# Kernel optimization log

Measured on AMD Instinct MI355X. Metric: run time of the kernel, lower is better.

The kernel has to match this reference:

```python
import jax, jax.numpy as jnp
import numpy as np
from jax import lax

B, CIN, COUT, H, W, K = 256, 512, 256, 8, 8, 8192


def setup_inputs() -> dict:
    key = jax.random.key(0)
    ks = jax.random.split(key, 6)
    scale = 0.05
    return {
        "latent": jax.random.normal(ks[0], (B, CIN, H, W), dtype=jnp.float32),
        "conv_w": jax.random.normal(ks[1], (COUT, CIN, 3, 3), dtype=jnp.float32) * scale,
        "conv_b": jax.random.normal(ks[2], (COUT,), dtype=jnp.float32) * scale,
        "lin_w": jax.random.normal(ks[3], (COUT, COUT), dtype=jnp.float32) * scale,
        "lin_b": jax.random.normal(ks[4], (COUT,), dtype=jnp.float32) * scale,
        "emb": jax.random.normal(ks[5], (K, COUT), dtype=jnp.float32),
    }


def reference(latent, conv_w, conv_b, lin_w, lin_b, emb):
    # pre-quantization conv: 3x3, stride 1, padding 1 (SAME), NCHW / OIHW
    x = lax.conv_general_dilated(
        latent, conv_w, window_strides=(1, 1), padding="SAME",
        dimension_numbers=("NCHW", "OIHW", "NCHW"),
    ) + conv_b[None, :, None, None]
    # permute(0,2,3,1) then linear on last dim
    x = jnp.transpose(x, (0, 2, 3, 1))              # [B,H,W,C]
    x = jnp.einsum("bhwc,dc->bhwd", x, lin_w) + lin_b
    flat = x.reshape(-1, x.shape[-1])               # [B*H*W, C]
    distances = (
        jnp.sum(flat ** 2, axis=1, keepdims=True)
        + jnp.sum(emb ** 2, axis=1)
        - 2.0 * flat @ emb.T
    )                                               # [B*H*W, K]
    encoding_indices = jnp.argmin(distances, axis=1)
    return encoding_indices.reshape(-1, 64)
```

## Files before the change

### kernel.cpp

```cpp
#include <hip/hip_runtime.h>
#include <cstdint>
#include <cstddef>


#define CIN_  512
#define E_    4608
#define M_    16384

typedef _Float16 half4_t __attribute__((ext_vector_type(4)));
typedef _Float16 half8_t __attribute__((ext_vector_type(8)));
typedef float f32x4 __attribute__((ext_vector_type(4)));

#define GLOAD_LDS16(gptr, lptr)                                         \
    __builtin_amdgcn_global_load_lds(                                   \
        (const __attribute__((address_space(1))) unsigned int*)(gptr),  \
        (__attribute__((address_space(3))) unsigned int*)(lptr), 16, 0, 0)

__global__ __launch_bounds__(256) void prep_k(
    const float* __restrict__ lat, const float* __restrict__ lin_w,
    const float* __restrict__ conv_w, const float* __restrict__ conv_b,
    const float* __restrict__ lin_b,
    _Float16* __restrict__ Xnp, _Float16* __restrict__ W2x,
    float* __restrict__ b2) {
    __shared__ float ls[8448];
    int bb = blockIdx.x, t = threadIdx.x;

    if (bb < 256) {
        float (*lt)[65] = (float(*)[65])ls;
        const float* src = lat + (size_t)bb * 512 * 64;
        _Float16* dst = Xnp + (size_t)bb * 64 * 1024;
        for (int c0 = 0; c0 < 512; c0 += 128) {
            __syncthreads();
            #pragma unroll
            for (int j = 0; j < 8; ++j) {
                int f4 = t + j * 256;
                int cc = f4 >> 4, p4 = (f4 & 15) * 4;
                float4 v = *(const float4*)(src + (size_t)(c0 + cc) * 64 + p4);
                lt[cc][p4] = v.x; lt[cc][p4 + 1] = v.y;
                lt[cc][p4 + 2] = v.z; lt[cc][p4 + 3] = v.w;
            }
            __syncthreads();
            int pix = t >> 2, cr = (t & 3) * 32;
            #pragma unroll
            for (int q = 0; q < 4; ++q) {
                half8_t hh, ll;
                #pragma unroll
                for (int j = 0; j < 8; ++j) {
                    float v = lt[cr + q * 8 + j][pix];
                    _Float16 h = (_Float16)v;
                    hh[j] = h; ll[j] = (_Float16)(v - (float)h);
                }
                *(half8_t*)(dst + (size_t)pix * 1024 + c0 + cr + q * 8) = hh;
                *(half8_t*)(dst + (size_t)pix * 1024 + 512 + c0 + cr + q * 8) = ll;
            }
        }
    } else if (bb < 832) {
        float (*lw)[33] = (float(*)[33])ls;
        int e0 = (bb - 256) * 8;
        int d = t;
        float acc[8];
        #pragma unroll
        for (int j = 0; j < 8; ++j) acc[j] = 0.f;
        for (int c0 = 0; c0 < 256; c0 += 32) {
            __syncthreads();
            #pragma unroll
            for (int k = 0; k < 8; ++k) {
                int f4 = t + k * 256;
                int row = f4 >> 3, c4 = (f4 & 7) * 4;
                float4 v = *(const float4*)(lin_w + (size_t)row * 256 + c0 + c4);
                lw[row][c4] = v.x; lw[row][c4 + 1] = v.y;
                lw[row][c4 + 2] = v.z; lw[row][c4 + 3] = v.w;
            }
            __syncthreads();
            for (int cp = 0; cp < 32; ++cp) {
                float lwv = lw[d][cp];
                const float* cwr = conv_w + (size_t)(c0 + cp) * E_ + e0;
                #pragma unroll
                for (int j = 0; j < 8; ++j) acc[j] += cwr[j] * lwv;
            }
        }
        #pragma unroll
        for (int j = 0; j < 8; ++j) {
            int e = e0 + j;
            int c = e / 9, t9 = e - c * 9;
            _Float16 h = (_Float16)acc[j];
            _Float16 l = (_Float16)(acc[j] - (float)h);
            W2x[((size_t)(t9 * 256 + d)) * 512 + c] = h;
            W2x[((size_t)((9 + t9) * 256 + d)) * 512 + c] = l;
        }
    } else {
        float (*lw)[33] = (float(*)[33])ls;
        int d = t;
        float acc = lin_b[d];
        for (int c0 = 0; c0 < 256; c0 += 32) {
            __syncthreads();
            #pragma unroll
            for (int k = 0; k < 8; ++k) {
                int f4 = t + k * 256;
                int row = f4 >> 3, c4 = (f4 & 7) * 4;
                float4 v = *(const float4*)(lin_w + (size_t)row * 256 + c0 + c4);
                lw[row][c4] = v.x; lw[row][c4 + 1] = v.y;
                lw[row][c4 + 2] = v.z; lw[row][c4 + 3] = v.w;
            }
            __syncthreads();
            for (int cp = 0; cp < 32; ++cp) acc += lw[d][cp] * conv_b[c0 + cp];
        }
        b2[d] = acc;
    }
}

__global__ __launch_bounds__(256) void convm8_k(
    const _Float16* __restrict__ Xnp, const _Float16* __restrict__ W2x,
    const float* __restrict__ b2, float* __restrict__ yb,
    float* __restrict__ tmp) {
    __shared__ char sm[65536];
    int m0 = blockIdx.x * 128, n0 = blockIdx.y * 128;
    int cc0 = blockIdx.z * 8;
    int tid = threadIdx.x, w = tid >> 6, lane = tid & 63;
    int wm = w & 1, wn = w >> 1;
    int fr = lane & 15, fq = lane >> 4;

    int xq = (fq ^ ((fr >> 1) & 3)) << 4;
    int boff[4];
    #pragma unroll
    for (int i = 0; i < 4; ++i) boff[i] = (wn * 64 + i * 16 + fr) * 64 + xq;
    int imgoff[4], ph[4], pw[4];
    #pragma unroll
    for (int s = 0; s < 4; ++s) {
        int rr = wm * 64 + s * 16 + fr;
        imgoff[s] = rr & 64; ph[s] = (rr >> 3) & 7; pw[s] = rr & 7;
    }
    int slt[2], sr[2], sq[2];
    #pragma unroll
    for (int i = 0; i < 2; ++i) {
        int s = w * 128 + i * 64 + lane;
        slt[i] = s;
        sr[i] = s >> 2;
        sq[i] = ((s & 3) ^ ((s >> 3) & 3)) * 8;
    }

    auto stageA = [&](int cc, int buf) {
        char* L = sm + buf * 16384;
        #pragma unroll
        for (int i = 0; i < 2; ++i) {
            const _Float16* base =
                Xnp + (size_t)(m0 + sr[i]) * 1024 + cc * 32 + sq[i];
            GLOAD_LDS16(base, L + slt[i] * 16);
            GLOAD_LDS16(base + 512, L + 8192 + slt[i] * 16);
        }
    };
    auto stageB = [&](int tap, int cc, int buf) {
        char* L = sm + 32768 + buf * 16384;
        #pragma unroll
        for (int i = 0; i < 2; ++i) {
            const _Float16* bb =
                W2x + ((size_t)(tap * 256 + n0 + sr[i])) * 512 + cc * 32 + sq[i];
            GLOAD_LDS16(bb, L + slt[i] * 16);
            GLOAD_LDS16(bb + (size_t)9 * 256 * 512, L + 8192 + slt[i] * 16);
        }
    };

    f32x4 acc[4][4];
    #pragma unroll
    for (int s = 0; s < 4; ++s)
        #pragma unroll
        for (int t = 0; t < 4; ++t)
            #pragma unroll
            for (int r = 0; r < 4; ++r) acc[s][t][r] = 0.f;

    stageA(cc0, 0);
    stageB(0, cc0, 0);
    const half8_t zfrag = {};
    int gi = 0;
    for (int cci = 0; cci < 8; ++cci) {
        int cc = cc0 + cci;
        const char* Ab = sm + (cci & 1) * 16384;
        for (int tap = 0; tap < 9; ++tap, ++gi) {
            __syncthreads();
            if (tap < 8) stageB(tap + 1, cc, (gi + 1) & 1);
            else if (cci < 7) stageB(0, cc + 1, (gi + 1) & 1);
            if (tap == 7 && cci < 7) stageA(cc + 1, (cci + 1) & 1);

            int dy = tap / 3 - 1, dx = tap - (tap / 3) * 3 - 1;
            half8_t ah[4], al[4];
            #pragma unroll
            for (int s = 0; s < 4; ++s) {
                int ih = ph[s] + dy, iw = pw[s] + dx;
                bool v = ((unsigned)ih < 8u) && ((unsigned)iw < 8u);
                int pp = imgoff[s] + (v ? ih * 8 + iw : 0);
                int ao = pp * 64 + ((fq ^ ((pp >> 1) & 3)) << 4);
                half8_t a0 = *(const half8_t*)(Ab + ao);
                half8_t a1 = *(const half8_t*)(Ab + 8192 + ao);
                ah[s] = v ? a0 : zfrag;
                al[s] = v ? a1 : zfrag;
            }
            const char* Bb = sm + 32768 + (gi & 1) * 16384;
            half8_t bh[4], bl[4];
            #pragma unroll
            for (int t = 0; t < 4; ++t) {
                bh[t] = *(const half8_t*)(Bb + boff[t]);
                bl[t] = *(const half8_t*)(Bb + 8192 + boff[t]);
            }
            #pragma unroll
            for (int s = 0; s < 4; ++s)
                #pragma unroll
                for (int t = 0; t < 4; ++t)
                    acc[s][t] = __builtin_amdgcn_mfma_f32_16x16x32_f16(
                        ah[s], bh[t], acc[s][t], 0, 0, 0);
            #pragma unroll
            for (int s = 0; s < 4; ++s)
                #pragma unroll
                for (int t = 0; t < 4; ++t)
                    acc[s][t] = __builtin_amdgcn_mfma_f32_16x16x32_f16(
                        ah[s], bl[t], acc[s][t], 0, 0, 0);
            #pragma unroll
            for (int s = 0; s < 4; ++s)
                #pragma unroll
                for (int t = 0; t < 4; ++t)
                    acc[s][t] = __builtin_amdgcn_mfma_f32_16x16x32_f16(
                        al[s], bh[t], acc[s][t], 0, 0, 0);
        }
    }

    float* dst = (blockIdx.z == 0) ? yb : tmp;
    float bv[4];
    #pragma unroll
    for (int t = 0; t < 4; ++t)
        bv[t] = (blockIdx.z == 0) ? b2[n0 + wn * 64 + t * 16 + fr] : 0.f;
    #pragma unroll
    for (int s = 0; s < 4; ++s)
        #pragma unroll
        for (int r = 0; r < 4; ++r) {
            int m = m0 + wm * 64 + s * 16 + fq * 4 + r;
            #pragma unroll
            for (int t = 0; t < 4; ++t) {
                int d = n0 + wn * 64 + t * 16 + fr;
                dst[(size_t)m * 256 + d] = acc[s][t][r] + bv[t];
            }
        }
}

__global__ __launch_bounds__(256) void pack3_k(
    float* __restrict__ yb, const float* __restrict__ tmp,
    const float* __restrict__ emb,
    _Float16* __restrict__ A2, _Float16* __restrict__ B2,
    float* __restrict__ esq) {
    #pragma unroll
    for (int it = 0; it < 8; ++it) {
        int i = (blockIdx.x + it * 512) * 256 + threadIdx.x;
        float4 v = *(const float4*)(yb + (size_t)i * 4);
        float4 t = *(const float4*)(tmp + (size_t)i * 4);
        float4 s = {v.x + t.x, v.y + t.y, v.z + t.z, v.w + t.w};
        *(float4*)(yb + (size_t)i * 4) = s;
        half4_t h = {(_Float16)s.x, (_Float16)s.y, (_Float16)s.z, (_Float16)s.w};
        *(half4_t*)(A2 + (size_t)i * 4) = h;
    }
    int w = threadIdx.x >> 6, lane = threadIdx.x & 63;
    #pragma unroll
    for (int j = 0; j < 4; ++j) {
        int k = blockIdx.x * 16 + w * 4 + j;
        float4 v = *(const float4*)(emb + (size_t)k * 256 + lane * 4);
        half4_t h = {(_Float16)v.x, (_Float16)v.y, (_Float16)v.z, (_Float16)v.w};
        *(half4_t*)(B2 + (size_t)k * 256 + lane * 4) = h;
        float s = v.x * v.x + v.y * v.y + v.z * v.z + v.w * v.w;
        #pragma unroll
        for (int m = 32; m >= 1; m >>= 1) s += __shfl_xor(s, m, 64);
        if (lane == 0) esq[k] = s;
    }
}

__global__ __launch_bounds__(512) void screen11_k(
    const _Float16* __restrict__ A2, const _Float16* __restrict__ B2,
    const float* __restrict__ esq, float* __restrict__ ps2, int* __restrict__ pi2) {
    __shared__ char sm[49152];
    int Lb = blockIdx.x;
    int xcd = Lb & 7, j = Lb >> 3;
    int mt = xcd * 16 + (j & 15);
    int nt = j >> 4;
    int m0 = mt * 128, n0 = nt * 256;
    int tid = threadIdx.x, w = tid >> 6, lane = tid & 63;
    int wm = w & 1, wn = w >> 1;
    int fr = lane & 15, fq = lane >> 4;

    int xq = (fq ^ ((fr >> 1) & 3)) << 4;
    int aoff[4], boff[4];
    #pragma unroll
    for (int i = 0; i < 4; ++i) {
        aoff[i] = (wm * 64 + i * 16 + fr) * 64 + xq;
        boff[i] = (wn * 64 + i * 16 + fr) * 64 + xq;
    }
    int sAr = tid >> 2, sAq = ((tid & 3) ^ ((tid >> 3) & 3)) * 8;
    int sBs[2], sBr[2], sBq[2];
    #pragma unroll
    for (int i = 0; i < 2; ++i) {
        int s = i * 512 + tid;
        sBs[i] = s;
        sBr[i] = s >> 2;
        sBq[i] = ((s & 3) ^ ((s >> 3) & 3)) * 8;
    }

    auto stage = [&](int kt, int buf) {
        char* L = sm + buf * 24576;
        int ko = kt * 32;
        GLOAD_LDS16(A2 + (size_t)(m0 + sAr) * 256 + ko + sAq, L + tid * 16);
        #pragma unroll
        for (int i = 0; i < 2; ++i)
            GLOAD_LDS16(B2 + (size_t)(n0 + sBr[i]) * 256 + ko + sBq[i],
                        L + 8192 + sBs[i] * 16);
    };

    f32x4 acc[4][4];
    #pragma unroll
    for (int s = 0; s < 4; ++s)
        #pragma unroll
        for (int t = 0; t < 4; ++t)
            #pragma unroll
            for (int r = 0; r < 4; ++r) acc[s][t][r] = 0.f;

    stage(0, 0);
    for (int kt = 0; kt < 8; ++kt) {
        __syncthreads();
        if (kt + 1 < 8) stage(kt + 1, (kt + 1) & 1);
        const char* L = sm + (kt & 1) * 24576;
        half8_t af[4], bf[4];
        #pragma unroll
        for (int s = 0; s < 4; ++s) af[s] = *(const half8_t*)(L + aoff[s]);
        #pragma unroll
        for (int t = 0; t < 4; ++t) bf[t] = *(const half8_t*)(L + 8192 + boff[t]);
        #pragma unroll
        for (int s = 0; s < 4; ++s)
            #pragma unroll
            for (int t = 0; t < 4; ++t)
                acc[s][t] = __builtin_amdgcn_mfma_f32_16x16x32_f16(
                    af[s], bf[t], acc[s][t], 0, 0, 0);
    }

    float esv[4];
    #pragma unroll
    for (int t = 0; t < 4; ++t) esv[t] = esq[n0 + wn * 64 + t * 16 + fr];
    int colIdx = nt * 4 + wn;
    #pragma unroll
    for (int s = 0; s < 4; ++s) {
        #pragma unroll
        for (int r = 0; r < 4; ++r) {
            float best = 3.4e38f; int bidx = 0x7fffffff;
            #pragma unroll
            for (int t = 0; t < 4; ++t) {
                float sc = esv[t] - 2.f * acc[s][t][r];
                int k = n0 + wn * 64 + t * 16 + fr;
                if (sc < best || (sc == best && k < bidx)) { best = sc; bidx = k; }
            }
            #pragma unroll
            for (int msk = 1; msk <= 8; msk <<= 1) {
                float so = __shfl_xor(best, msk, 64);
                int ko2 = __shfl_xor(bidx, msk, 64);
                if (so < best || (so == best && ko2 < bidx)) { best = so; bidx = ko2; }
            }
            if (fr == 0) {
                int m = m0 + wm * 64 + s * 16 + fq * 4 + r;
                ps2[(size_t)m * 128 + colIdx] = best;
                pi2[(size_t)m * 128 + colIdx] = bidx;
            }
        }
    }
}

__global__ __launch_bounds__(256) void refine3_k(
    const float* __restrict__ y, const float* __restrict__ emb,
    const float* __restrict__ esq, const float* __restrict__ ps2,
    const int* __restrict__ pi2, int* __restrict__ out) {
    int lane = threadIdx.x & 63;
    for (int j = 0; j < 8; ++j) {
        int m = blockIdx.x * 32 + j * 4 + (threadIdx.x >> 6);
        float4 yv = *(const float4*)(y + (size_t)m * 256 + lane * 4);
        float sc_[2]; int kc_[2];
        #pragma unroll
        for (int i = 0; i < 2; ++i) {
            sc_[i] = ps2[(size_t)m * 128 + lane * 2 + i];
            kc_[i] = pi2[(size_t)m * 128 + lane * 2 + i];
        }
        float s0 = fminf(sc_[0], sc_[1]);
        #pragma unroll
        for (int msk = 1; msk <= 32; msk <<= 1) s0 = fminf(s0, __shfl_xor(s0, msk, 64));
        float thr = s0 + 0.25f;
        float best = 3.4e38f; int bk = 0x7fffffff;
        for (int c = 0; c < 128; ++c) {
            float scc = __shfl(sc_[c & 1], c >> 1, 64);
            if (scc <= thr) {
                int k = __shfl(kc_[c & 1], c >> 1, 64);
                float4 ev = *(const float4*)(emb + (size_t)k * 256 + lane * 4);
                float d = yv.x * ev.x + yv.y * ev.y + yv.z * ev.z + yv.w * ev.w;
                #pragma unroll
                for (int msk = 1; msk <= 32; msk <<= 1) d += __shfl_xor(d, msk, 64);
                float sx = esq[k] - 2.f * d;
                if (sx < best || (sx == best && k < bk)) { best = sx; bk = k; }
            }
        }
        if (lane == 0) out[m] = bk;
    }
}

extern "C" void kernel_launch(void* const* d_in, const int* in_sizes, int n_in,
                              void* d_out, int out_size, void* d_ws, size_t ws_size,
                              hipStream_t stream) {
    const float* latent = (const float*)d_in[0];
    const float* conv_w = (const float*)d_in[1];
    const float* conv_b = (const float*)d_in[2];
    const float* lin_w  = (const float*)d_in[3];
    const float* lin_b  = (const float*)d_in[4];
    const float* emb    = (const float*)d_in[5];
    int* out = (int*)d_out;

    char* W = (char*)d_ws;
    float*    b2  = (float*)(W + 262144);
    float*    esq = (float*)(W + 263168);
    float*    yb  = (float*)(W + 295936);
    _Float16* W2x = (_Float16*)(W + 17073152);
    _Float16* Xnp = (_Float16*)(W + 21792768);
    _Float16* A2  = (_Float16*)(W + 21792768);
    _Float16* B2  = (_Float16*)(W + 30181376);
    float*    ps2 = (float*)(W + 34375680);
    int*      pi2 = (int*)(W + 42764288);
    float*    tmp = (float*)(W + 34375680);

    prep_k<<<833, 256, 0, stream>>>(latent, lin_w, conv_w, conv_b, lin_b,
                                    Xnp, W2x, b2);
    convm8_k<<<dim3(128, 2, 2), 256, 0, stream>>>(Xnp, W2x, b2, yb, tmp);
    pack3_k<<<512, 256, 0, stream>>>(yb, tmp, emb, A2, B2, esq);
    screen11_k<<<4096, 512, 0, stream>>>(A2, B2, esq, ps2, pi2);
    refine3_k<<<512, 256, 0, stream>>>(yb, emb, esq, ps2, pi2, out);
}
```

Before: 440.3 us.

## Merge conv N-tiles into 512-thread blocks sharing A tile; split screen launch

```diff
diff --git a/kernel.cpp b/kernel.cpp
--- a/kernel.cpp
+++ b/kernel.cpp
@@ -109,15 +109,16 @@
     }
 }
 
-__global__ __launch_bounds__(256) void convm8_k(
+__global__ __launch_bounds__(512) void convm9_k(
     const _Float16* __restrict__ Xnp, const _Float16* __restrict__ W2x,
     const float* __restrict__ b2, float* __restrict__ yb,
     float* __restrict__ tmp) {
-    __shared__ char sm[65536];
-    int m0 = blockIdx.x * 128, n0 = blockIdx.y * 128;
-    int cc0 = blockIdx.z * 8;
+    __shared__ char sm[98304];
+    int m0 = blockIdx.x * 128;
+    int cc0 = blockIdx.y * 8;
     int tid = threadIdx.x, w = tid >> 6, lane = tid & 63;
-    int wm = w & 1, wn = w >> 1;
+    int wm = w & 1, wn = w >> 2;
+    wn = (w >> 1);
     int fr = lane & 15, fq = lane >> 4;
 
     int xq = (fq ^ ((fr >> 1) & 3)) << 4;
@@ -130,33 +131,31 @@
         int rr = wm * 64 + s * 16 + fr;
         imgoff[s] = rr & 64; ph[s] = (rr >> 3) & 7; pw[s] = rr & 7;
     }
-    int slt[2], sr[2], sq[2];
+    int sAr = tid >> 2, sAq = ((tid & 3) ^ ((tid >> 3) & 3)) * 8;
+    int sBs[2], sBr[2], sBq[2];
     #pragma unroll
     for (int i = 0; i < 2; ++i) {
-        int s = w * 128 + i * 64 + lane;
-        slt[i] = s;
-        sr[i] = s >> 2;
-        sq[i] = ((s & 3) ^ ((s >> 3) & 3)) * 8;
+        int s = i * 512 + tid;
+        sBs[i] = s;
+        sBr[i] = s >> 2;
+        sBq[i] = ((s & 3) ^ ((s >> 3) & 3)) * 8;
     }
 
     auto stageA = [&](int cc, int buf) {
         char* L = sm + buf * 16384;
-        #pragma unroll
-        for (int i = 0; i < 2; ++i) {
-            const _Float16* base =
-                Xnp + (size_t)(m0 + sr[i]) * 1024 + cc * 32 + sq[i];
-            GLOAD_LDS16(base, L + slt[i] * 16);
-            GLOAD_LDS16(base + 512, L + 8192 + slt[i] * 16);
-        }
+        const _Float16* base =
+            Xnp + (size_t)(m0 + sAr) * 1024 + cc * 32 + sAq;
+        GLOAD_LDS16(base, L + tid * 16);
+        GLOAD_LDS16(base + 512, L + 8192 + tid * 16);
     };
     auto stageB = [&](int tap, int cc, int buf) {
-        char* L = sm + 32768 + buf * 16384;
+        char* L = sm + 32768 + buf * 32768;
         #pragma unroll
         for (int i = 0; i < 2; ++i) {
             const _Float16* bb =
-                W2x + ((size_t)(tap * 256 + n0 + sr[i])) * 512 + cc * 32 + sq[i];
-            GLOAD_LDS16(bb, L + slt[i] * 16);
-            GLOAD_LDS16(bb + (size_t)9 * 256 * 512, L + 8192 + slt[i] * 16);
+                W2x + ((size_t)(tap * 256 + sBr[i])) * 512 + cc * 32 + sBq[i];
+            GLOAD_LDS16(bb, L + sBs[i] * 16);
+            GLOAD_LDS16(bb + (size_t)9 * 256 * 512, L + 16384 + sBs[i] * 16);
         }
     };
 
@@ -194,12 +193,12 @@
                 ah[s] = v ? a0 : zfrag;
                 al[s] = v ? a1 : zfrag;
             }
-            const char* Bb = sm + 32768 + (gi & 1) * 16384;
+            const char* Bb = sm + 32768 + (gi & 1) * 32768;
             half8_t bh[4], bl[4];
             #pragma unroll
             for (int t = 0; t < 4; ++t) {
                 bh[t] = *(const half8_t*)(Bb + boff[t]);
-                bl[t] = *(const half8_t*)(Bb + 8192 + boff[t]);
+                bl[t] = *(const half8_t*)(Bb + 16384 + boff[t]);
             }
             #pragma unroll
             for (int s = 0; s < 4; ++s)
@@ -222,11 +221,11 @@
         }
     }
 
-    float* dst = (blockIdx.z == 0) ? yb : tmp;
+    float* dst = (blockIdx.y == 0) ? yb : tmp;
     float bv[4];
     #pragma unroll
     for (int t = 0; t < 4; ++t)
-        bv[t] = (blockIdx.z == 0) ? b2[n0 + wn * 64 + t * 16 + fr] : 0.f;
+        bv[t] = (blockIdx.y == 0) ? b2[wn * 64 + t * 16 + fr] : 0.f;
     #pragma unroll
     for (int s = 0; s < 4; ++s)
         #pragma unroll
@@ -234,7 +233,7 @@
             int m = m0 + wm * 64 + s * 16 + fq * 4 + r;
             #pragma unroll
             for (int t = 0; t < 4; ++t) {
-                int d = n0 + wn * 64 + t * 16 + fr;
+                int d = wn * 64 + t * 16 + fr;
                 dst[(size_t)m * 256 + d] = acc[s][t][r] + bv[t];
             }
         }
@@ -271,9 +270,10 @@
 
 __global__ __launch_bounds__(512) void screen11_k(
     const _Float16* __restrict__ A2, const _Float16* __restrict__ B2,
-    const float* __restrict__ esq, float* __restrict__ ps2, int* __restrict__ pi2) {
+    const float* __restrict__ esq, float* __restrict__ ps2, int* __restrict__ pi2,
+    int off) {
     __shared__ char sm[49152];
-    int Lb = blockIdx.x;
+    int Lb = blockIdx.x + off;
     int xcd = Lb & 7, j = Lb >> 3;
     int mt = xcd * 16 + (j & 15);
     int nt = j >> 4;
@@ -425,8 +425,11 @@
 
     prep_k<<<833, 256, 0, stream>>>(latent, lin_w, conv_w, conv_b, lin_b,
                                     Xnp, W2x, b2);
-    convm8_k<<<dim3(128, 2, 2), 256, 0, stream>>>(Xnp, W2x, b2, yb, tmp);
+    convm9_k<<<dim3(128, 2), 512, 0, stream>>>(Xnp, W2x, b2, yb, tmp);
     pack3_k<<<512, 256, 0, stream>>>(yb, tmp, emb, A2, B2, esq);
-    screen11_k<<<4096, 512, 0, stream>>>(A2, B2, esq, ps2, pi2);
+    screen11_k<<<1024, 512, 0, stream>>>(A2, B2, esq, ps2, pi2, 0);
+    screen11_k<<<1024, 512, 0, stream>>>(A2, B2, esq, ps2, pi2, 1024);
+    screen11_k<<<1024, 512, 0, stream>>>(A2, B2, esq, ps2, pi2, 2048);
+    screen11_k<<<1024, 512, 0, stream>>>(A2, B2, esq, ps2, pi2, 3072);
     refine3_k<<<512, 256, 0, stream>>>(yb, emb, esq, ps2, pi2, out);
 }
```

Measured after the change: 471.2 us. 7.0% more time.
